# Performance work log

Measured on AMD Instinct MI355X. Metric: run time of the kernel, lower is better.

The kernel has to match this reference:

```python
import jax, jax.numpy as jnp
import numpy as np

EPS = 1e-3  # sscp_conv_group_norm_eps


def setup_inputs() -> dict:
    key = jax.random.key(0)
    k1, k2, k3 = jax.random.split(key, 3)
    audio_encodings = jax.random.normal(k1, (4, 1, 4096, 128), dtype=jnp.float32)
    # Conv2d(in=1, out=128, kernel=(3,3), stride=(2,2), bias=False), OIHW layout
    conv_w = jax.random.normal(k2, (128, 1, 3, 3), dtype=jnp.float32) * 0.1
    # AudioCumulativeGroupNorm per-channel scale (init ones; randomize slightly)
    norm_scale = jnp.ones((128,), dtype=jnp.float32) + 0.01 * jax.random.normal(k3, (128,), dtype=jnp.float32)
    return {"audio_encodings": audio_encodings, "conv_w": conv_w, "norm_scale": norm_scale}


def reference(audio_encodings, conv_w, norm_scale):
    # manual_padding = (0, 1, 1, 1) in torch F.pad order (W_left, W_right, H_top, H_bottom)
    x = jnp.pad(audio_encodings, ((0, 0), (0, 0), (1, 1), (0, 1)))
    # Conv2d stride (2,2), no padding, no bias
    y = jax.lax.conv_general_dilated(
        x, conv_w, window_strides=(2, 2), padding='VALID',
        dimension_numbers=('NCHW', 'OIHW', 'NCHW'))  # [B, C, T, F]
    # permute to [B, T, F, C] and normalize cumulatively over T (mask=None)
    h = jnp.transpose(y, (0, 2, 3, 1)).astype(jnp.float32)
    B, T, F, C = h.shape
    # cumulative count of elements per group at each t: (t+1) * F * C
    cnt = (jnp.arange(1, T + 1, dtype=jnp.float32) * (F * C)).reshape(1, T, 1, 1)
    cum_sum = jnp.cumsum(jnp.sum(h, axis=(2, 3), keepdims=True), axis=1)  # [B,T,1,1]
    cum_mean = cum_sum / cnt
    sq = jnp.sum((h - cum_mean) ** 2, axis=(2, 3), keepdims=True)
    cum_var = jnp.cumsum(sq, axis=1) / cnt
    normed = (h - cum_mean) * jax.lax.rsqrt(cum_var + EPS) * norm_scale  # scale per channel (last dim)
    out = jnp.transpose(normed, (0, 3, 1, 2))  # back to [B, C, T, F]
    return jax.nn.relu(out)
```

## Files before the change

### kernel.cpp

```cpp
#include <hip/hip_runtime.h>

#define X_H 4096
#define X_W 128
#define BATCH 4
#define CH 128
#define TT_OUT 2048
#define FF 64
#define EPS_GN 1e-3f

typedef float f4 __attribute__((ext_vector_type(4)));
typedef float f2 __attribute__((ext_vector_type(2)));

#define S1_OFF 0
#define SS_OFF (BATCH*TT_OUT)
#define MI_OFF (2*BATCH*TT_OUT)

__global__ __launch_bounds__(256) void stats_kernel(const float* __restrict__ x,
                                                    const float* __restrict__ w,
                                                    float* __restrict__ ws) {
    __shared__ float wlds[CH*9];
    __shared__ float Ml[81];
    __shared__ float Wl[9];
    int tid = threadIdx.x;
#pragma unroll
    for (int i = tid; i < CH*9; i += 256) wlds[i] = w[i];
    __syncthreads();
    if (tid < 81) {
        int j = tid / 9, k = tid % 9;
        float acc = 0.f;
#pragma unroll 8
        for (int c = 0; c < CH; ++c) acc = fmaf(wlds[c*9 + j], wlds[c*9 + k], acc);
        Ml[tid] = acc;
    } else if (tid < 90) {
        int k = tid - 81;
        float acc = 0.f;
#pragma unroll 8
        for (int c = 0; c < CH; ++c) acc += wlds[c*9 + k];
        Wl[k] = acc;
    }
    __syncthreads();

    int fq = tid & 15;
    int tr = tid >> 4;
    int gt = blockIdx.x * 16 + tr;
    int t = gt & (TT_OUT - 1);
    int b = gt >> 11;
    const float* xb = x + (size_t)b * (X_H * X_W);

    float xr[3][9];
    int r0 = 2*t - 1;
#pragma unroll
    for (int kh = 0; kh < 3; ++kh) {
        int r = r0 + kh;
        if (r >= 0 && r < X_H) {
            const float* rp = xb + (size_t)r * X_W + 8*fq;
            f4 v0 = *(const f4*)rp;
            f4 v1 = *(const f4*)(rp + 4);
            xr[kh][0]=v0.x; xr[kh][1]=v0.y; xr[kh][2]=v0.z; xr[kh][3]=v0.w;
            xr[kh][4]=v1.x; xr[kh][5]=v1.y; xr[kh][6]=v1.z; xr[kh][7]=v1.w;
            xr[kh][8] = (fq == 15) ? 0.f : rp[8];
        } else {
#pragma unroll
            for (int k = 0; k < 9; ++k) xr[kh][k] = 0.f;
        }
    }

    float s1 = 0.f, ss = 0.f;
#pragma unroll
    for (int jf = 0; jf < 4; ++jf) {
        float tv[9];
#pragma unroll
        for (int kh = 0; kh < 3; ++kh)
#pragma unroll
            for (int kw = 0; kw < 3; ++kw)
                tv[kh*3+kw] = xr[kh][2*jf + kw];
#pragma unroll
        for (int k = 0; k < 9; ++k) s1 = fmaf(Wl[k], tv[k], s1);
#pragma unroll
        for (int j = 0; j < 9; ++j) {
            float tj = 0.f;
#pragma unroll
            for (int k = 0; k < 9; ++k) tj = fmaf(Ml[j*9+k], tv[k], tj);
            ss = fmaf(tv[j], tj, ss);
        }
    }
#pragma unroll
    for (int off = 1; off < 16; off <<= 1) {
        s1 += __shfl_xor(s1, off);
        ss += __shfl_xor(ss, off);
    }
    if (fq == 0) {
        ws[S1_OFF + gt] = s1;
        ws[SS_OFF + gt] = ss;
    }
}

__global__ __launch_bounds__(256) void scan_kernel(float* __restrict__ ws) {
    int b = blockIdx.x;
    int tid = threadIdx.x;
    int lane = tid & 63;
    int wv = tid >> 6;
    const f4* S1v = (const f4*)(ws + S1_OFF + b*TT_OUT);
    const f4* SSv = (const f4*)(ws + SS_OFF + b*TT_OUT);
    f2* MI = (f2*)(ws + MI_OFF) + b*TT_OUT;
    __shared__ float wsum_lds[4];

    f4 a0 = S1v[tid*2], a1 = S1v[tid*2+1];
    f4 b0 = SSv[tid*2], b1 = SSv[tid*2+1];
    float s1loc[8] = {a0.x,a0.y,a0.z,a0.w,a1.x,a1.y,a1.z,a1.w};
    float ssloc[8] = {b0.x,b0.y,b0.z,b0.w,b1.x,b1.y,b1.z,b1.w};

    float v[8];
    float tot = 0.f;
#pragma unroll
    for (int i = 0; i < 8; ++i) { tot += s1loc[i]; v[i] = tot; }
    float incl = tot;
#pragma unroll
    for (int off = 1; off < 64; off <<= 1) {
        float n = __shfl_up(incl, off);
        if (lane >= off) incl += n;
    }
    if (lane == 63) wsum_lds[wv] = incl;
    __syncthreads();
    float woff = 0.f;
    for (int w2 = 0; w2 < wv; ++w2) woff += wsum_lds[w2];
    float prefix = woff + incl - tot;

    float muloc[8], v2[8];
    float tot2 = 0.f;
#pragma unroll
    for (int i = 0; i < 8; ++i) {
        int t = tid*8 + i;
        float cs = prefix + v[i];
        float cnt = (float)(t+1) * 8192.f;
        float mu = cs / cnt;
        float sq = ssloc[i] - 2.f*mu*s1loc[i] + 8192.f*mu*mu;
        muloc[i] = mu;
        tot2 += sq; v2[i] = tot2;
    }
    float incl2 = tot2;
#pragma unroll
    for (int off = 1; off < 64; off <<= 1) {
        float n = __shfl_up(incl2, off);
        if (lane >= off) incl2 += n;
    }
    __syncthreads();
    if (lane == 63) wsum_lds[wv] = incl2;
    __syncthreads();
    float woff2 = 0.f;
    for (int w2 = 0; w2 < wv; ++w2) woff2 += wsum_lds[w2];
    float prefix2 = woff2 + incl2 - tot2;
#pragma unroll
    for (int i = 0; i < 8; ++i) {
        int t = tid*8 + i;
        float cnt = (float)(t+1) * 8192.f;
        float var = (prefix2 + v2[i]) / cnt;
        f2 mi;
        mi.x = muloc[i];
        mi.y = rsqrtf(var + EPS_GN);
        MI[t] = mi;
    }
}

#define T_TILE 16
#define CG 32
__global__ __launch_bounds__(256) void out_kernel(const float* __restrict__ x,
        const float* __restrict__ w, const float* __restrict__ scale,
        const float* __restrict__ ws, float* __restrict__ out) {
    __shared__ float wl[CG][9];
    __shared__ float sl[CG];
    int tid = threadIdx.x;
    int b = blockIdx.z;
    int c0 = blockIdx.y * CG;
    int t0 = blockIdx.x * T_TILE;
    for (int i = tid; i < CG*9; i += 256) wl[i/9][i%9] = w[c0*9 + i];
    if (tid < CG) sl[tid] = scale[c0 + tid];
    __syncthreads();

    int fq = tid & 15;
    int tr = tid >> 4;
    int t = t0 + tr;
    const float* xb = x + (size_t)b * (X_H * X_W);
    f2 mi = ((const f2*)(ws + MI_OFF))[b*TT_OUT + t];
    float mu = mi.x, istd = mi.y;

    float xr[3][9];
    int r0 = 2*t - 1;
#pragma unroll
    for (int kh = 0; kh < 3; ++kh) {
        int r = r0 + kh;
        if (r >= 0 && r < X_H) {
            const float* rp = xb + (size_t)r * X_W + 8*fq;
            f4 v0 = *(const f4*)rp;
            f4 v1 = *(const f4*)(rp + 4);
            xr[kh][0]=v0.x; xr[kh][1]=v0.y; xr[kh][2]=v0.z; xr[kh][3]=v0.w;
            xr[kh][4]=v1.x; xr[kh][5]=v1.y; xr[kh][6]=v1.z; xr[kh][7]=v1.w;
            xr[kh][8] = (fq == 15) ? 0.f : rp[8];
        } else {
#pragma unroll
            for (int k = 0; k < 9; ++k) xr[kh][k] = 0.f;
        }
    }

    float* ob = out + (((size_t)(b*CH + c0) * TT_OUT + t) * FF + 4*fq);
#pragma unroll
    for (int c = 0; c < CG; ++c) {
        float a  = istd * sl[c];
        float nb = -mu * a;
        f4 v;
#pragma unroll
        for (int jf = 0; jf < 4; ++jf) {
            float h = 0.f;
#pragma unroll
            for (int kh = 0; kh < 3; ++kh)
#pragma unroll
                for (int kw = 0; kw < 3; ++kw)
                    h = fmaf(wl[c][kh*3+kw], xr[kh][2*jf + kw], h);
            v[jf] = fmaxf(fmaf(h, a, nb), 0.f);
        }
        __builtin_nontemporal_store(v, (f4*)(ob + (size_t)c * (TT_OUT * FF)));
    }
}

extern "C" void kernel_launch(void* const* d_in, const int* in_sizes, int n_in,
                              void* d_out, int out_size, void* d_ws, size_t ws_size,
                              hipStream_t stream) {
    const float* x     = (const float*)d_in[0];
    const float* w     = (const float*)d_in[1];
    const float* scale = (const float*)d_in[2];
    float* out = (float*)d_out;
    float* ws  = (float*)d_ws;

    stats_kernel<<<(BATCH*TT_OUT)/16, 256, 0, stream>>>(x, w, ws);
    scan_kernel<<<BATCH, 256, 0, stream>>>(ws);
    out_kernel<<<dim3(TT_OUT/T_TILE, CH/CG, BATCH), 256, 0, stream>>>(x, w, scale, ws, out);
}
```

Baseline: 65.60 us.

## Fuse cumulative-stat scan into output kernel, drop separate scan launch

Removes the standalone scan kernel and has every output block recompute the prefix sums of per-timestep sum and centered square sum up to its tile from the stats buffer, then run a serial 16-step scan inside the tile. This drops one kernel launch and the serialization of a 4-block scan, at the cost of redundant prefix work (2048 floats each) in every one of the 2048 output blocks. It also switches output stores from nontemporal to regular stores. The centered square sums are now summed in a different order, which slightly changes floating-point rounding.

```diff
diff --git a/kernel.cpp b/kernel.cpp
--- a/kernel.cpp
+++ b/kernel.cpp
@@ -9,11 +9,9 @@
 #define EPS_GN 1e-3f
 
 typedef float f4 __attribute__((ext_vector_type(4)));
-typedef float f2 __attribute__((ext_vector_type(2)));
 
 #define S1_OFF 0
 #define SS_OFF (BATCH*TT_OUT)
-#define MI_OFF (2*BATCH*TT_OUT)
 
 __global__ __launch_bounds__(256) void stats_kernel(const float* __restrict__ x,
                                                     const float* __restrict__ w,
@@ -95,73 +93,6 @@
     }
 }
 
-__global__ __launch_bounds__(256) void scan_kernel(float* __restrict__ ws) {
-    int b = blockIdx.x;
-    int tid = threadIdx.x;
-    int lane = tid & 63;
-    int wv = tid >> 6;
-    const f4* S1v = (const f4*)(ws + S1_OFF + b*TT_OUT);
-    const f4* SSv = (const f4*)(ws + SS_OFF + b*TT_OUT);
-    f2* MI = (f2*)(ws + MI_OFF) + b*TT_OUT;
-    __shared__ float wsum_lds[4];
-
-    f4 a0 = S1v[tid*2], a1 = S1v[tid*2+1];
-    f4 b0 = SSv[tid*2], b1 = SSv[tid*2+1];
-    float s1loc[8] = {a0.x,a0.y,a0.z,a0.w,a1.x,a1.y,a1.z,a1.w};
-    float ssloc[8] = {b0.x,b0.y,b0.z,b0.w,b1.x,b1.y,b1.z,b1.w};
-
-    float v[8];
-    float tot = 0.f;
-#pragma unroll
-    for (int i = 0; i < 8; ++i) { tot += s1loc[i]; v[i] = tot; }
-    float incl = tot;
-#pragma unroll
-    for (int off = 1; off < 64; off <<= 1) {
-        float n = __shfl_up(incl, off);
-        if (lane >= off) incl += n;
-    }
-    if (lane == 63) wsum_lds[wv] = incl;
-    __syncthreads();
-    float woff = 0.f;
-    for (int w2 = 0; w2 < wv; ++w2) woff += wsum_lds[w2];
-    float prefix = woff + incl - tot;
-
-    float muloc[8], v2[8];
-    float tot2 = 0.f;
-#pragma unroll
-    for (int i = 0; i < 8; ++i) {
-        int t = tid*8 + i;
-        float cs = prefix + v[i];
-        float cnt = (float)(t+1) * 8192.f;
-        float mu = cs / cnt;
-        float sq = ssloc[i] - 2.f*mu*s1loc[i] + 8192.f*mu*mu;
-        muloc[i] = mu;
-        tot2 += sq; v2[i] = tot2;
-    }
-    float incl2 = tot2;
-#pragma unroll
-    for (int off = 1; off < 64; off <<= 1) {
-        float n = __shfl_up(incl2, off);
-        if (lane >= off) incl2 += n;
-    }
-    __syncthreads();
-    if (lane == 63) wsum_lds[wv] = incl2;
-    __syncthreads();
-    float woff2 = 0.f;
-    for (int w2 = 0; w2 < wv; ++w2) woff2 += wsum_lds[w2];
-    float prefix2 = woff2 + incl2 - tot2;
-#pragma unroll
-    for (int i = 0; i < 8; ++i) {
-        int t = tid*8 + i;
-        float cnt = (float)(t+1) * 8192.f;
-        float var = (prefix2 + v2[i]) / cnt;
-        f2 mi;
-        mi.x = muloc[i];
-        mi.y = rsqrtf(var + EPS_GN);
-        MI[t] = mi;
-    }
-}
-
 #define T_TILE 16
 #define CG 32
 __global__ __launch_bounds__(256) void out_kernel(const float* __restrict__ x,
@@ -169,20 +100,85 @@
         const float* __restrict__ ws, float* __restrict__ out) {
     __shared__ float wl[CG][9];
     __shared__ float sl[CG];
+    __shared__ float redA[4], redB[4], redC[4];
     int tid = threadIdx.x;
+    int lane = tid & 63;
+    int wv = tid >> 6;
     int b = blockIdx.z;
     int c0 = blockIdx.y * CG;
     int t0 = blockIdx.x * T_TILE;
+
     for (int i = tid; i < CG*9; i += 256) wl[i/9][i%9] = w[c0*9 + i];
     if (tid < CG) sl[tid] = scale[c0 + tid];
-    __syncthreads();
+
+    const float* S1 = ws + S1_OFF + b*TT_OUT;
+    const float* SS = ws + SS_OFF + b*TT_OUT;
+    const f4* S1v = (const f4*)S1;
+    const f4* SSv = (const f4*)SS;
+    f4 a0 = S1v[tid*2], a1 = S1v[tid*2+1];
+    f4 e0 = SSv[tid*2], e1 = SSv[tid*2+1];
+    float s1l[8] = {a0.x,a0.y,a0.z,a0.w,a1.x,a1.y,a1.z,a1.w};
+    float ssl[8] = {e0.x,e0.y,e0.z,e0.w,e1.x,e1.y,e1.z,e1.w};
+    int tau0 = tid * 8;
+    float s1m[8];
+    float tot = 0.f;
+#pragma unroll
+    for (int i = 0; i < 8; ++i) {
+        s1m[i] = (tau0 + i < t0) ? s1l[i] : 0.f;
+        tot += s1m[i];
+    }
+    float incl = tot;
+#pragma unroll
+    for (int off = 1; off < 64; off <<= 1) {
+        float n = __shfl_up(incl, off);
+        if (lane >= off) incl += n;
+    }
+    if (lane == 63) redA[wv] = incl;
+    __syncthreads();
+    float woff = 0.f;
+    for (int w2 = 0; w2 < wv; ++w2) woff += redA[w2];
+    float prefix = woff + incl - tot;
+
+    float run = prefix;
+    float sqp = 0.f;
+#pragma unroll
+    for (int i = 0; i < 8; ++i) {
+        if (tau0 + i < t0) {
+            run += s1l[i];
+            float cnt = (float)(tau0 + i + 1) * 8192.f;
+            float mu = run / cnt;
+            sqp += ssl[i] - 2.f*mu*s1l[i] + 8192.f*mu*mu;
+        }
+    }
+    float r1 = tot, r2 = sqp;
+#pragma unroll
+    for (int off = 32; off > 0; off >>= 1) {
+        r1 += __shfl_xor(r1, off);
+        r2 += __shfl_xor(r2, off);
+    }
+    if (lane == 0) { redB[wv] = r1; redC[wv] = r2; }
+    __syncthreads();
+    float base1 = redB[0] + redB[1] + redB[2] + redB[3];
+    float base_sq = redC[0] + redC[1] + redC[2] + redC[3];
+
+    int tr = tid >> 4;
+    float run16 = base1, sq16 = base_sq;
+    float mu_t = 0.f, istd_t = 0.f;
+#pragma unroll
+    for (int i = 0; i < T_TILE; ++i) {
+        int t = t0 + i;
+        float s1t = S1[t];
+        float sst = SS[t];
+        run16 += s1t;
+        float cnt = (float)(t + 1) * 8192.f;
+        float mu = run16 / cnt;
+        sq16 += sst - 2.f*mu*s1t + 8192.f*mu*mu;
+        if (i == tr) { mu_t = mu; istd_t = rsqrtf(sq16 / cnt + EPS_GN); }
+    }
 
     int fq = tid & 15;
-    int tr = tid >> 4;
     int t = t0 + tr;
     const float* xb = x + (size_t)b * (X_H * X_W);
-    f2 mi = ((const f2*)(ws + MI_OFF))[b*TT_OUT + t];
-    float mu = mi.x, istd = mi.y;
 
     float xr[3][9];
     int r0 = 2*t - 1;
@@ -205,8 +201,8 @@
     float* ob = out + (((size_t)(b*CH + c0) * TT_OUT + t) * FF + 4*fq);
 #pragma unroll
     for (int c = 0; c < CG; ++c) {
-        float a  = istd * sl[c];
-        float nb = -mu * a;
+        float a  = istd_t * sl[c];
+        float nb = -mu_t * a;
         f4 v;
 #pragma unroll
         for (int jf = 0; jf < 4; ++jf) {
@@ -218,7 +214,7 @@
                     h = fmaf(wl[c][kh*3+kw], xr[kh][2*jf + kw], h);
             v[jf] = fmaxf(fmaf(h, a, nb), 0.f);
         }
-        __builtin_nontemporal_store(v, (f4*)(ob + (size_t)c * (TT_OUT * FF)));
+        *(f4*)(ob + (size_t)c * (TT_OUT * FF)) = v;
     }
 }
 
@@ -232,6 +228,5 @@
     float* ws  = (float*)d_ws;
 
     stats_kernel<<<(BATCH*TT_OUT)/16, 256, 0, stream>>>(x, w, ws);
-    scan_kernel<<<BATCH, 256, 0, stream>>>(ws);
     out_kernel<<<dim3(TT_OUT/T_TILE, CH/CG, BATCH), 256, 0, stream>>>(x, w, scale, ws, out);
 }
```

Result: faster. 59.35 us (-9.5%).
